# Performance work log

Hardware: AMD Instinct MI355X
Metric: run time of the kernel (lower is better)

The kernel has to match this reference:

```python
import jax, jax.numpy as jnp
import numpy as np

E = 1024
H = 16
DH = E // H
LN_EPS = 1e-5


def setup_inputs() -> dict:
    key = jax.random.key(0)
    ks = jax.random.split(key, 9)
    B, Lq, Lk = 8, 1024, 1024
    s = 0.02
    return {
        "query": jax.random.normal(ks[0], (B, Lq, E), jnp.float32),
        "key_t": jax.random.normal(ks[1], (B, Lk, E), jnp.float32),
        "value": jax.random.normal(ks[2], (B, Lk, E), jnp.float32),
        "in_proj_w": jax.random.normal(ks[3], (3 * E, E), jnp.float32) * s,
        "in_proj_b": jnp.zeros((3 * E,), jnp.float32),
        "out_proj_w": jax.random.normal(ks[4], (E, E), jnp.float32) * s,
        "out_proj_b": jnp.zeros((E,), jnp.float32),
        "ln_gamma": jnp.ones((E,), jnp.float32),
        "ln_beta": jnp.zeros((E,), jnp.float32),
    }


def _mha_cross(query, key_t, value, in_proj_w, in_proj_b, out_proj_w, out_proj_b,
               ln_gamma, ln_beta):
    B, Lq, _ = query.shape
    Lk = key_t.shape[1]
    wq, wk, wv = in_proj_w[:E], in_proj_w[E:2 * E], in_proj_w[2 * E:]
    bq, bk, bv = in_proj_b[:E], in_proj_b[E:2 * E], in_proj_b[2 * E:]
    # projections (torch Linear: x @ W^T + b)
    q = (query @ wq.T + bq).reshape(B, Lq, H, DH)
    k = (key_t @ wk.T + bk).reshape(B, Lk, H, DH)
    v = (value @ wv.T + bv).reshape(B, Lk, H, DH)
    scale = 1.0 / np.sqrt(DH).astype(np.float32)
    # unfused attention: explicit [B,H,Lq,Lk] scores (need_weights=True path)
    scores = jnp.einsum("bqhd,bkhd->bhqk", q, k) * scale
    probs = jax.nn.softmax(scores, axis=-1)
    attn = jnp.einsum("bhqk,bkhd->bqhd", probs, v).reshape(B, Lq, E)
    attn_out = attn @ out_proj_w.T + out_proj_b
    # averaged attention weights (average_attn_weights=True default)
    attn_weights = probs.mean(axis=1)  # [B, Lq, Lk]
    # residual + LayerNorm
    x = query + attn_out
    mu = x.mean(axis=-1, keepdims=True)
    var = x.var(axis=-1, keepdims=True)
    y = (x - mu) * jax.lax.rsqrt(var + LN_EPS) * ln_gamma + ln_beta
    return y, attn_weights


def reference(query, key_t, value, in_proj_w, in_proj_b, out_proj_w, out_proj_b,
              ln_gamma, ln_beta):
    return _mha_cross(query, key_t, value, in_proj_w, in_proj_b,
                      out_proj_w, out_proj_b, ln_gamma, ln_beta)
```

## Files before the change

kernel.cpp:

```cpp
#include <hip/hip_runtime.h>
#include <stdint.h>

#define E_DIM 1024
#define H_NUM 16
#define B_NUM 8
#define LQ 1024
#define LK 1024
#define MROWS (B_NUM * LQ)

typedef unsigned short u16;
typedef __attribute__((ext_vector_type(8))) short bf16x8;
typedef __attribute__((ext_vector_type(4))) short bf16x4;
typedef __attribute__((ext_vector_type(4))) float f32x4;
typedef bf16x8 __attribute__((may_alias)) bf16x8_ma;
typedef bf16x4 __attribute__((may_alias)) bf16x4_ma;

typedef __attribute__((address_space(1))) const void* gas_ptr;
typedef __attribute__((address_space(3))) void* las_ptr;

__device__ __forceinline__ void gload16(const void* g, void* l) {
  __builtin_amdgcn_global_load_lds((gas_ptr)g, (las_ptr)l, 16, 0, 0);
}

__device__ __forceinline__ u16 f2bf(float f) {
  union { float f; uint32_t u; } c; c.f = f;
  return (u16)((c.u + 0x7FFFu + ((c.u >> 16) & 1u)) >> 16);
}

#define MFMA_BF16(a, b, c) __builtin_amdgcn_mfma_f32_16x16x32_bf16((a), (b), (c), 0, 0, 0)

#define SCALE_Q 0.18033688011112042f

__global__ __launch_bounds__(256) void cvt_f32_bf16(const float* __restrict__ src,
                                                    u16* __restrict__ dst, int n4) {
  int i = blockIdx.x * 256 + threadIdx.x;
  const int stride = gridDim.x * 256;
  for (; i < n4; i += stride) {
    float4 v = ((const float4*)src)[i];
    ushort4 o;
    o.x = f2bf(v.x); o.y = f2bf(v.y); o.z = f2bf(v.z); o.w = f2bf(v.w);
    ((ushort4*)dst)[i] = o;
  }
}

__global__ __launch_bounds__(256) void cvt3_f32_bf16(
    const float* __restrict__ a0, const float* __restrict__ a1, const float* __restrict__ a2,
    u16* __restrict__ o0, u16* __restrict__ o1, u16* __restrict__ o2, int n4) {
  const float* s = (blockIdx.y == 0) ? a0 : (blockIdx.y == 1 ? a1 : a2);
  u16* d = (blockIdx.y == 0) ? o0 : (blockIdx.y == 1 ? o1 : o2);
  int i = blockIdx.x * 256 + threadIdx.x;
  const int stride = gridDim.x * 256;
  for (; i < n4; i += stride) {
    float4 v = ((const float4*)s)[i];
    ushort4 o;
    o.x = f2bf(v.x); o.y = f2bf(v.y); o.z = f2bf(v.z); o.w = f2bf(v.w);
    ((ushort4*)d)[i] = o;
  }
}

template <int MODE>
__global__ __launch_bounds__(256) void gemm_bt(
    const u16* __restrict__ A0, const u16* __restrict__ A1, const u16* __restrict__ A2,
    const u16* __restrict__ W, const float* __restrict__ bias,
    const float* __restrict__ resid,
    u16* __restrict__ outb, float* __restrict__ outf,
    int N, int K, int nwg_n, int nwg_m) {
  __shared__ u16 As[128 * 64];
  __shared__ u16 Bs[128 * 64];

  const int tid = threadIdx.x;
  const int wave = tid >> 6;
  const int lane = tid & 63;
  const int lr = lane & 15, lg = lane >> 4;
  const int wr = wave >> 1, wc = wave & 1;

  const int cpx = (int)gridDim.x >> 3;
  const int bid = blockIdx.x;
  const int wg = (bid & 7) * cpx + (bid >> 3);
  const int n_i = wg % nwg_n;
  const int rest = wg / nwg_n;
  const int m_i = rest % nwg_m;
  const int z = rest / nwg_m;

  const int m0 = m_i * 128;
  const int n0 = n_i * 128;

  const u16* Az = (z == 0) ? A0 : (z == 1 ? A1 : A2);
  const u16* Wz = W + (size_t)z * N * K;
  const float* bs = bias + z * N;
  const float scale = (MODE == 0 && z == 0) ? SCALE_Q : 1.0f;

  const f32x4 fzero = {0.f, 0.f, 0.f, 0.f};
  f32x4 acc[4][4];
#pragma unroll
  for (int a = 0; a < 4; ++a)
#pragma unroll
    for (int b = 0; b < 4; ++b) acc[a][b] = fzero;

  const int lrow8 = lane >> 3;
  const int lcol8 = (lane & 7) * 8;

  for (int kt = 0; kt < K; kt += 64) {
#pragma unroll
    for (int i = 0; i < 4; ++i) {
      const int seg = i * 4 + wave;
      gload16(Wz + (size_t)(n0 + seg * 8 + lrow8) * K + kt + lcol8, &Bs[seg * 512]);
      gload16(Az + (size_t)(m0 + seg * 8 + lrow8) * K + kt + lcol8, &As[seg * 512]);
    }
    __syncthreads();

#pragma unroll
    for (int kk = 0; kk < 64; kk += 32) {
      bf16x8 av[4], bv[4];
#pragma unroll
      for (int t = 0; t < 4; ++t)
        av[t] = *(const bf16x8*)&As[(wr * 64 + t * 16 + lr) * 64 + kk + lg * 8];
#pragma unroll
      for (int t = 0; t < 4; ++t)
        bv[t] = *(const bf16x8*)&Bs[(wc * 64 + t * 16 + lr) * 64 + kk + lg * 8];
#pragma unroll
      for (int mi = 0; mi < 4; ++mi)
#pragma unroll
        for (int ni = 0; ni < 4; ++ni)
          acc[mi][ni] = MFMA_BF16(av[mi], bv[ni], acc[mi][ni]);
    }
    __syncthreads();
  }

  float bvv[4];
#pragma unroll
  for (int ni = 0; ni < 4; ++ni) bvv[ni] = bs[n0 + wc * 64 + ni * 16 + lr];

  if (MODE == 0) {
    u16* Cb = outb + (size_t)z * (size_t)MROWS * N;
#pragma unroll
    for (int mi = 0; mi < 4; ++mi) {
#pragma unroll
      for (int i = 0; i < 4; ++i) {
        const size_t m = (size_t)(m0 + wr * 64 + mi * 16 + lg * 4 + i);
#pragma unroll
        for (int ni = 0; ni < 4; ++ni) {
          const int n = n0 + wc * 64 + ni * 16 + lr;
          Cb[m * N + n] = f2bf((acc[mi][ni][i] + bvv[ni]) * scale);
        }
      }
    }
  } else {
#pragma unroll
    for (int mi = 0; mi < 4; ++mi) {
#pragma unroll
      for (int i = 0; i < 4; ++i) {
        const size_t m = (size_t)(m0 + wr * 64 + mi * 16 + lg * 4 + i);
#pragma unroll
        for (int ni = 0; ni < 4; ++ni) {
          const int n = n0 + wc * 64 + ni * 16 + lr;
          outf[m * N + n] = acc[mi][ni][i] + bvv[ni] + resid[m * N + n];
        }
      }
    }
  }
}

__global__ __launch_bounds__(256) void transpose_v(const u16* __restrict__ Vb,
                                                   u16* __restrict__ Vtg) {
  __shared__ u16 T[64 * 264];
  const int tid = threadIdx.x;
  const int b = blockIdx.z, h = blockIdx.y;
  const int k0 = blockIdx.x * 256;
  const int bh = b * H_NUM + h;
  const int krow = tid >> 3;
  const int d0 = (tid & 7) * 8;
  const int jst = krow & 7;
#pragma unroll
  for (int it = 0; it < 8; ++it) {
    const int k = it * 32 + krow;
    bf16x8 v = *(const bf16x8*)&Vb[(size_t)(b * LK + k0 + k) * E_DIM + h * 64 + d0];
#pragma unroll
    for (int jj = 0; jj < 8; ++jj) {
      const int j = (jj + jst) & 7;
      T[(d0 + j) * 264 + k] = (u16)v[j];
    }
  }
  __syncthreads();
  const int d = tid >> 2;
  const int kk0 = (tid & 3) * 64;
  u16* orow = &Vtg[(size_t)(bh * 64 + d) * LK + k0 + kk0];
#pragma unroll
  for (int c = 0; c < 8; ++c)
    *(bf16x8*)&orow[c * 8] = *(const bf16x8*)&T[d * 264 + kk0 + c * 8];
}

__global__ __launch_bounds__(256) void attn_fwd(
    const u16* __restrict__ Qb, const u16* __restrict__ Kb, const u16* __restrict__ Vtg,
    u16* __restrict__ attnb, float* __restrict__ denom) {
  __shared__ u16 Ks[64 * 72];
  __shared__ u16 Vt[64 * 72];
  __shared__ u16 Pw[4][16 * 72];

  const int tid = threadIdx.x;
  const int wave = tid >> 6, lane = tid & 63;
  const int lr = lane & 15, lg = lane >> 4;

  const int bid = blockIdx.x;
  const int wg = (bid & 7) * 256 + (bid >> 3);
  const int qt = wg & 15;
  const int h = (wg >> 4) & 15;
  const int b = wg >> 8;
  const int bh = b * H_NUM + h;
  const int q0 = qt * 64;

  const size_t qoff = (size_t)(b * LQ + q0 + wave * 16 + lr) * E_DIM + h * 64;
  const bf16x8 qf0 = *(const bf16x8*)&Qb[qoff + lg * 8];
  const bf16x8 qf1 = *(const bf16x8*)&Qb[qoff + 32 + lg * 8];

  const f32x4 fzero = {0.f, 0.f, 0.f, 0.f};
  f32x4 ctx[4];
#pragma unroll
  for (int d = 0; d < 4; ++d) ctx[d] = fzero;
  float dnl = 0.f;

  const int sr = tid >> 2;
  const int sc = (tid & 3) * 16;
  const u16* Kg = &Kb[(size_t)(b * LK + sr) * E_DIM + h * 64 + sc];
  const u16* Vg = &Vtg[(size_t)(bh * 64 + sr) * LK + sc];

  bf16x8 kr0 = *(const bf16x8*)(Kg);
  bf16x8 kr1 = *(const bf16x8*)(Kg + 8);
  bf16x8 vr0 = *(const bf16x8*)(Vg);
  bf16x8 vr1 = *(const bf16x8*)(Vg + 8);
  *(bf16x8*)&Ks[sr * 72 + sc] = kr0; *(bf16x8*)&Ks[sr * 72 + sc + 8] = kr1;
  *(bf16x8*)&Vt[sr * 72 + sc] = vr0; *(bf16x8*)&Vt[sr * 72 + sc + 8] = vr1;

  for (int t = 0; t < 16; ++t) {
    __syncthreads();
    if (t < 15) {
      const int k1 = (t + 1) * 64;
      kr0 = *(const bf16x8*)(Kg + (size_t)k1 * E_DIM);
      kr1 = *(const bf16x8*)(Kg + (size_t)k1 * E_DIM + 8);
      vr0 = *(const bf16x8*)(Vg + k1);
      vr1 = *(const bf16x8*)(Vg + k1 + 8);
    }
#pragma unroll
    for (int kf = 0; kf < 4; ++kf) {
      const bf16x8 kb0 = *(const bf16x8*)&Ks[(kf * 16 + lr) * 72 + lg * 8];
      const bf16x8 kb1 = *(const bf16x8*)&Ks[(kf * 16 + lr) * 72 + 32 + lg * 8];
      f32x4 s = fzero;
      s = MFMA_BF16(kb0, qf0, s);
      s = MFMA_BF16(kb1, qf1, s);
      const float p0 = exp2f(s[0]), p1 = exp2f(s[1]);
      const float p2 = exp2f(s[2]), p3 = exp2f(s[3]);
      dnl += (p0 + p1) + (p2 + p3);
      bf16x4 w;
      w[0] = (short)f2bf(p0); w[1] = (short)f2bf(p1);
      w[2] = (short)f2bf(p2); w[3] = (short)f2bf(p3);
      *(bf16x4_ma*)&Pw[wave][lr * 72 + kf * 16 + lg * 4] = w;
    }
    const bf16x8 pa0 = *(const bf16x8_ma*)&Pw[wave][lr * 72 + lg * 8];
    const bf16x8 pa1 = *(const bf16x8_ma*)&Pw[wave][lr * 72 + 32 + lg * 8];
#pragma unroll
    for (int df = 0; df < 4; ++df) {
      const bf16x8 vb0 = *(const bf16x8*)&Vt[(df * 16 + lr) * 72 + lg * 8];
      const bf16x8 vb1 = *(const bf16x8*)&Vt[(df * 16 + lr) * 72 + 32 + lg * 8];
      ctx[df] = MFMA_BF16(pa0, vb0, ctx[df]);
      ctx[df] = MFMA_BF16(pa1, vb1, ctx[df]);
    }
    __syncthreads();
    if (t < 15) {
      *(bf16x8*)&Ks[sr * 72 + sc] = kr0; *(bf16x8*)&Ks[sr * 72 + sc + 8] = kr1;
      *(bf16x8*)&Vt[sr * 72 + sc] = vr0; *(bf16x8*)&Vt[sr * 72 + sc + 8] = vr1;
    }
  }

  dnl += __shfl_xor(dnl, 16, 64);
  dnl += __shfl_xor(dnl, 32, 64);
  if (lane < 16) denom[(size_t)bh * LQ + q0 + wave * 16 + lane] = dnl;
  float dnv[4];
#pragma unroll
  for (int i = 0; i < 4; ++i) dnv[i] = __shfl(dnl, lg * 4 + i, 64);

#pragma unroll
  for (int i = 0; i < 4; ++i) {
    const float inv = 1.0f / dnv[i];
    const int q = q0 + wave * 16 + lg * 4 + i;
    const size_t orow = (size_t)(b * LQ + q) * E_DIM + h * 64;
#pragma unroll
    for (int df = 0; df < 4; ++df)
      attnb[orow + df * 16 + lr] = f2bf(ctx[df][i] * inv);
  }
}

__global__ __launch_bounds__(256) void attn_wts(
    const u16* __restrict__ Qb, const u16* __restrict__ Kb,
    const float* __restrict__ denom, float* __restrict__ aw) {
  __shared__ u16 Ks[128 * 72];

  const int tid = threadIdx.x;
  const int wave = tid >> 6, lane = tid & 63;
  const int lr = lane & 15, lg = lane >> 4;

  const int bid = blockIdx.x;
  const int wg = (bid & 7) * 128 + (bid >> 3);
  const int q0 = (wg & 15) * 64;
  const int k0 = ((wg >> 4) & 7) * 128;
  const int b = wg >> 7;

  const f32x4 fzero = {0.f, 0.f, 0.f, 0.f};
  f32x4 acc[2][4];
#pragma unroll
  for (int t = 0; t < 2; ++t)
#pragma unroll
    for (int f = 0; f < 4; ++f) acc[t][f] = fzero;

  const int sr = tid >> 1;
  const int sc = (tid & 1) * 32;
  const u16* Kg = &Kb[(size_t)(b * LK + k0 + sr) * E_DIM + sc];
  const size_t qbase = (size_t)(b * LQ + q0 + wave * 16 + lr) * E_DIM;
  const size_t dbase = (size_t)(b * H_NUM) * LQ + q0 + wave * 16 + lg * 4;

  bf16x8 r0 = *(const bf16x8*)(Kg);
  bf16x8 r1 = *(const bf16x8*)(Kg + 8);
  bf16x8 r2 = *(const bf16x8*)(Kg + 16);
  bf16x8 r3 = *(const bf16x8*)(Kg + 24);
  *(bf16x8*)&Ks[sr * 72 + sc] = r0;      *(bf16x8*)&Ks[sr * 72 + sc + 8] = r1;
  *(bf16x8*)&Ks[sr * 72 + sc + 16] = r2; *(bf16x8*)&Ks[sr * 72 + sc + 24] = r3;

  for (int h = 0; h < H_NUM; ++h) {
    __syncthreads();
    if (h < 15) {
      const u16* Kn = Kg + (h + 1) * 64;
      r0 = *(const bf16x8*)(Kn);
      r1 = *(const bf16x8*)(Kn + 8);
      r2 = *(const bf16x8*)(Kn + 16);
      r3 = *(const bf16x8*)(Kn + 24);
    }
    const bf16x8 qf0 = *(const bf16x8*)&Qb[qbase + h * 64 + lg * 8];
    const bf16x8 qf1 = *(const bf16x8*)&Qb[qbase + h * 64 + 32 + lg * 8];
    float rd[4];
#pragma unroll
    for (int i = 0; i < 4; ++i)
      rd[i] = 0.0625f / denom[dbase + (size_t)h * LQ + i];

#pragma unroll
    for (int kt = 0; kt < 2; ++kt) {
#pragma unroll
      for (int f = 0; f < 4; ++f) {
        const int row = kt * 64 + f * 16 + lr;
        const bf16x8 kb0 = *(const bf16x8*)&Ks[row * 72 + lg * 8];
        const bf16x8 kb1 = *(const bf16x8*)&Ks[row * 72 + 32 + lg * 8];
        f32x4 s = fzero;
        s = MFMA_BF16(qf0, kb0, s);
        s = MFMA_BF16(qf1, kb1, s);
#pragma unroll
        for (int i = 0; i < 4; ++i)
          acc[kt][f][i] += exp2f(s[i]) * rd[i];
      }
    }
    __syncthreads();
    if (h < 15) {
      *(bf16x8*)&Ks[sr * 72 + sc] = r0;      *(bf16x8*)&Ks[sr * 72 + sc + 8] = r1;
      *(bf16x8*)&Ks[sr * 72 + sc + 16] = r2; *(bf16x8*)&Ks[sr * 72 + sc + 24] = r3;
    }
  }

#pragma unroll
  for (int kt = 0; kt < 2; ++kt)
#pragma unroll
    for (int f = 0; f < 4; ++f)
#pragma unroll
      for (int i = 0; i < 4; ++i) {
        const int q = q0 + wave * 16 + lg * 4 + i;
        aw[(size_t)(b * LQ + q) * LK + k0 + kt * 64 + f * 16 + lr] = acc[kt][f][i];
      }
}

__global__ __launch_bounds__(256) void ln_kernel(float* __restrict__ xy,
                                                 const float* __restrict__ gamma,
                                                 const float* __restrict__ beta) {
  __shared__ float ls[4], ls2[4];
  const int row = blockIdx.x;
  const int tid = threadIdx.x;
  float4* xr = (float4*)(xy + (size_t)row * E_DIM);
  float4 v = xr[tid];
  float s = v.x + v.y + v.z + v.w;
  float s2 = v.x * v.x + v.y * v.y + v.z * v.z + v.w * v.w;
#pragma unroll
  for (int off = 32; off >= 1; off >>= 1) {
    s += __shfl_xor(s, off, 64);
    s2 += __shfl_xor(s2, off, 64);
  }
  const int wave = tid >> 6, lane = tid & 63;
  if (lane == 0) { ls[wave] = s; ls2[wave] = s2; }
  __syncthreads();
  s = ls[0] + ls[1] + ls[2] + ls[3];
  s2 = ls2[0] + ls2[1] + ls2[2] + ls2[3];
  const float mu = s * (1.0f / E_DIM);
  const float var = s2 * (1.0f / E_DIM) - mu * mu;
  const float rs = rsqrtf(var + 1e-5f);
  const float4 g = ((const float4*)gamma)[tid];
  const float4 bt = ((const float4*)beta)[tid];
  float4 o;
  o.x = (v.x - mu) * rs * g.x + bt.x;
  o.y = (v.y - mu) * rs * g.y + bt.y;
  o.z = (v.z - mu) * rs * g.z + bt.z;
  o.w = (v.w - mu) * rs * g.w + bt.w;
  xr[tid] = o;
}

extern "C" void kernel_launch(void* const* d_in, const int* in_sizes, int n_in,
                              void* d_out, int out_size, void* d_ws, size_t ws_size,
                              hipStream_t stream) {
  (void)in_sizes; (void)n_in; (void)out_size; (void)ws_size;
  const float* query     = (const float*)d_in[0];
  const float* key_t     = (const float*)d_in[1];
  const float* value     = (const float*)d_in[2];
  const float* in_proj_b = (const float*)d_in[4];
  const float* out_proj_b = (const float*)d_in[6];
  const float* ln_gamma  = (const float*)d_in[7];
  const float* ln_beta   = (const float*)d_in[8];

  float* y  = (float*)d_out;
  float* aw = y + (size_t)B_NUM * LQ * E_DIM;

  const size_t SZ = (size_t)B_NUM * LQ * E_DIM;
  u16* ws    = (u16*)d_ws;
  u16* Qb    = ws;
  u16* Kb    = ws + SZ;
  u16* Vb    = ws + 2 * SZ;
  u16* attnb = ws + 3 * SZ;
  u16* wqkvb = ws + 4 * SZ;
  u16* woutb = wqkvb + 3 * E_DIM * E_DIM;
  float* denom = (float*)(wqkvb + 4 * (size_t)E_DIM * E_DIM);

  u16* Xq  = (u16*)aw;
  u16* Xk  = Xq + SZ;
  u16* Xv  = (u16*)y;
  u16* Vtg = (u16*)y;

  cvt_f32_bf16<<<3072, 256, 0, stream>>>((const float*)d_in[3], wqkvb, (3 * E_DIM * E_DIM) / 4);
  cvt_f32_bf16<<<1024, 256, 0, stream>>>((const float*)d_in[5], woutb, (E_DIM * E_DIM) / 4);
  cvt3_f32_bf16<<<dim3(2048, 3), 256, 0, stream>>>(query, key_t, value, Xq, Xk, Xv, (int)(SZ / 4));

  gemm_bt<0><<<1536, 256, 0, stream>>>(
      Xq, Xk, Xv, wqkvb, in_proj_b, nullptr, Qb, nullptr, E_DIM, E_DIM, 8, 64);

  transpose_v<<<dim3(4, 16, 8), 256, 0, stream>>>(Vb, Vtg);

  attn_fwd<<<2048, 256, 0, stream>>>(Qb, Kb, Vtg, attnb, denom);

  attn_wts<<<1024, 256, 0, stream>>>(Qb, Kb, denom, aw);

  gemm_bt<1><<<512, 256, 0, stream>>>(
      attnb, attnb, attnb, woutb, out_proj_b, query, nullptr, y, E_DIM, E_DIM, 8, 64);

  ln_kernel<<<8192, 256, 0, stream>>>(y, ln_gamma, ln_beta);
}
```

Baseline: 309.1 us.

## Replace 128x128 GEMM with pipelined 256x256 tile, swizzled LDS, 8 waves

Replaces the projection and output GEMMs with a 256x256-tile, 512-thread kernel. It double-buffers K=64 slices in 128KB of LDS with an XOR-swizzled layout, and interleaves async global-to-LDS loads with MFMA phases, using explicit waitcnt, barriers and setprio. The aim is to raise arithmetic intensity and hide load latency behind the matrix ops. In exchange the out-projection launches only 128 workgroups, which may underfill the GPU, and the fine-grained barrier and waitcnt choreography is fragile.

```diff
diff --git a/kernel.cpp b/kernel.cpp
--- a/kernel.cpp
+++ b/kernel.cpp
@@ -58,21 +58,56 @@
   }
 }
 
+
+#define BAR() __builtin_amdgcn_s_barrier()
+#define LGKM0() do { asm volatile("s_waitcnt lgkmcnt(0)" ::: "memory"); \
+                     __builtin_amdgcn_sched_barrier(0); } while (0)
+#define LGKM8() asm volatile("s_waitcnt lgkmcnt(8)" ::: "memory")
+#define VMC(n) asm volatile("s_waitcnt vmcnt(" n ")" ::: "memory")
+
+#define STAGEH(mat, rowbase, kt, ldsoff)                                     \
+  { const u16* _s = (mat) + (size_t)(rowbase) * E_DIM + (kt);                \
+    gload16(_s + goff0, ldsv + (ldsoff) + wave * 1024);                      \
+    gload16(_s + goff1, ldsv + (ldsoff) + 8192 + wave * 1024); }
+
+#define READ_B(db)                                                           \
+  _Pragma("unroll") for (int n = 0; n < 4; ++n) {                            \
+    const int rgb = wn4 + n;                                                 \
+    _Pragma("unroll") for (int ks = 0; ks < 2; ++ks)                         \
+      bfr[n][ks] = *(const bf16x8_ma*)(ldsc + 65536 + (db) * 32768 +         \
+          ((rgb >> 3) << 14) + (((rgb & 7) * 2 + ks) << 10) + lanebase);     \
+  }
+
+#define READ_A(db, q)                                                        \
+  _Pragma("unroll") for (int jj = 0; jj < 2; ++jj) {                         \
+    const int rga = 4 * (q) + 2 * jj + wm;                                   \
+    _Pragma("unroll") for (int ks = 0; ks < 2; ++ks)                         \
+      afr[jj][ks] = *(const bf16x8_ma*)(ldsc + (db) * 32768 +                \
+          ((rga >> 3) << 14) + (((rga & 7) * 2 + ks) << 10) + lanebase);     \
+  }
+
+#define MMA(q)                                                               \
+  __builtin_amdgcn_s_setprio(1);                                             \
+  _Pragma("unroll") for (int jj = 0; jj < 2; ++jj)                           \
+    _Pragma("unroll") for (int n = 0; n < 4; ++n)                            \
+      _Pragma("unroll") for (int ks = 0; ks < 2; ++ks)                       \
+        acc[2 * (q) + jj][n] =                                               \
+            MFMA_BF16(afr[jj][ks], bfr[n][ks], acc[2 * (q) + jj][n]);        \
+  __builtin_amdgcn_s_setprio(0);
+
 template <int MODE>
-__global__ __launch_bounds__(256) void gemm_bt(
+__global__ __launch_bounds__(512, 2) void gemm256(
     const u16* __restrict__ A0, const u16* __restrict__ A1, const u16* __restrict__ A2,
     const u16* __restrict__ W, const float* __restrict__ bias,
     const float* __restrict__ resid,
     u16* __restrict__ outb, float* __restrict__ outf,
-    int N, int K, int nwg_n, int nwg_m) {
-  __shared__ u16 As[128 * 64];
-  __shared__ u16 Bs[128 * 64];
+    int nwg_n, int nwg_m) {
+  __shared__ u16 lds[65536];
 
   const int tid = threadIdx.x;
-  const int wave = tid >> 6;
-  const int lane = tid & 63;
+  const int wave = tid >> 6, lane = tid & 63;
   const int lr = lane & 15, lg = lane >> 4;
-  const int wr = wave >> 1, wc = wave & 1;
+  const int wm = wave >> 2, wn4 = (wave & 3) * 4;
 
   const int cpx = (int)gridDim.x >> 3;
   const int bid = blockIdx.x;
@@ -81,80 +116,132 @@
   const int rest = wg / nwg_n;
   const int m_i = rest % nwg_m;
   const int z = rest / nwg_m;
-
-  const int m0 = m_i * 128;
-  const int n0 = n_i * 128;
+  const int m0 = m_i * 256, n0 = n_i * 256;
 
   const u16* Az = (z == 0) ? A0 : (z == 1 ? A1 : A2);
-  const u16* Wz = W + (size_t)z * N * K;
-  const float* bs = bias + z * N;
+  const u16* Wz = W + (size_t)z * E_DIM * E_DIM;
+  const float* bs = bias + z * E_DIM;
   const float scale = (MODE == 0 && z == 0) ? SCALE_Q : 1.0f;
 
+  int goff0, goff1;
+  {
+    const int X0 = wave * 1024 + lane * 16;
+    const int L0 = X0 ^ (((X0 >> 9) & 1) << 5);
+    goff0 = (((L0 >> 10) >> 1) * 16 + ((L0 >> 6) & 15)) * E_DIM +
+            ((L0 >> 10) & 1) * 32 + ((L0 & 63) >> 1);
+    const int X1 = 8192 + X0;
+    const int L1 = X1 ^ (((X1 >> 9) & 1) << 5);
+    goff1 = (((L1 >> 10) >> 1) * 16 + ((L1 >> 6) & 15)) * E_DIM +
+            ((L1 >> 10) & 1) * 32 + ((L1 & 63) >> 1);
+  }
+  const char* ldsc = (const char*)lds;
+  char* ldsv = (char*)lds;
+  const int lanebase = lr * 64 + ((lg * 16) ^ ((lane & 8) << 2));
+
   const f32x4 fzero = {0.f, 0.f, 0.f, 0.f};
-  f32x4 acc[4][4];
-#pragma unroll
-  for (int a = 0; a < 4; ++a)
-#pragma unroll
-    for (int b = 0; b < 4; ++b) acc[a][b] = fzero;
-
-  const int lrow8 = lane >> 3;
-  const int lcol8 = (lane & 7) * 8;
-
-  for (int kt = 0; kt < K; kt += 64) {
-#pragma unroll
-    for (int i = 0; i < 4; ++i) {
-      const int seg = i * 4 + wave;
-      gload16(Wz + (size_t)(n0 + seg * 8 + lrow8) * K + kt + lcol8, &Bs[seg * 512]);
-      gload16(Az + (size_t)(m0 + seg * 8 + lrow8) * K + kt + lcol8, &As[seg * 512]);
-    }
-    __syncthreads();
-
-#pragma unroll
-    for (int kk = 0; kk < 64; kk += 32) {
-      bf16x8 av[4], bv[4];
-#pragma unroll
-      for (int t = 0; t < 4; ++t)
-        av[t] = *(const bf16x8*)&As[(wr * 64 + t * 16 + lr) * 64 + kk + lg * 8];
-#pragma unroll
-      for (int t = 0; t < 4; ++t)
-        bv[t] = *(const bf16x8*)&Bs[(wc * 64 + t * 16 + lr) * 64 + kk + lg * 8];
-#pragma unroll
-      for (int mi = 0; mi < 4; ++mi)
-#pragma unroll
-        for (int ni = 0; ni < 4; ++ni)
-          acc[mi][ni] = MFMA_BF16(av[mi], bv[ni], acc[mi][ni]);
-    }
-    __syncthreads();
+  f32x4 acc[8][4];
+#pragma unroll
+  for (int j = 0; j < 8; ++j)
+#pragma unroll
+    for (int n = 0; n < 4; ++n) acc[j][n] = fzero;
+
+  STAGEH(Az, m0,       0,  0);
+  STAGEH(Az, m0 + 128, 0,  16384);
+  STAGEH(Wz, n0,       0,  65536);
+  STAGEH(Wz, n0 + 128, 0,  65536 + 16384);
+  STAGEH(Wz, n0,       64, 65536 + 32768);
+  STAGEH(Wz, n0 + 128, 64, 65536 + 32768 + 16384);
+  STAGEH(Az, m0,       64, 32768);
+  VMC("6");
+  BAR();
+
+  bf16x8 bfr[4][2], afr[2][2];
+#pragma unroll 1
+  for (int i = 0; i < 8; ++i) {
+    const int kt2 = i * 128 + 128;
+    const bool nl = (i < 7);
+    READ_B(0) READ_A(0, 0)
+    STAGEH(Az, m0 + 128, i * 128 + 64, 32768 + 16384);
+    LGKM8();
+    BAR(); LGKM0();
+    MMA(0)
+    BAR();
+    READ_A(0, 1)
+    if (nl) STAGEH(Wz, n0, kt2, 65536);
+    BAR(); LGKM0();
+    MMA(1)
+    BAR();
+    READ_A(0, 2)
+    if (nl) STAGEH(Az, m0, kt2, 0);
+    BAR(); LGKM0();
+    MMA(2)
+    BAR();
+    READ_A(0, 3)
+    if (nl) {
+      STAGEH(Wz, n0 + 128, kt2, 65536 + 16384);
+      VMC("6");
+    } else {
+      VMC("0");
+    }
+    BAR(); LGKM0();
+    MMA(3)
+    BAR();
+    READ_B(1) READ_A(1, 0)
+    if (nl) STAGEH(Az, m0 + 128, kt2, 16384);
+    LGKM8();
+    BAR(); LGKM0();
+    MMA(0)
+    BAR();
+    READ_A(1, 1)
+    if (nl) STAGEH(Wz, n0, kt2 + 64, 65536 + 32768);
+    BAR(); LGKM0();
+    MMA(1)
+    BAR();
+    READ_A(1, 2)
+    if (nl) STAGEH(Wz, n0 + 128, kt2 + 64, 65536 + 32768 + 16384);
+    BAR(); LGKM0();
+    MMA(2)
+    BAR();
+    READ_A(1, 3)
+    if (nl) {
+      STAGEH(Az, m0, kt2 + 64, 32768);
+      VMC("6");
+    }
+    BAR(); LGKM0();
+    MMA(3)
+    BAR();
   }
 
   float bvv[4];
 #pragma unroll
-  for (int ni = 0; ni < 4; ++ni) bvv[ni] = bs[n0 + wc * 64 + ni * 16 + lr];
+  for (int n = 0; n < 4; ++n) bvv[n] = bs[n0 + wn4 * 16 + n * 16 + lr];
 
   if (MODE == 0) {
-    u16* Cb = outb + (size_t)z * (size_t)MROWS * N;
-#pragma unroll
-    for (int mi = 0; mi < 4; ++mi) {
-#pragma unroll
-      for (int i = 0; i < 4; ++i) {
-        const size_t m = (size_t)(m0 + wr * 64 + mi * 16 + lg * 4 + i);
-#pragma unroll
-        for (int ni = 0; ni < 4; ++ni) {
-          const int n = n0 + wc * 64 + ni * 16 + lr;
-          Cb[m * N + n] = f2bf((acc[mi][ni][i] + bvv[ni]) * scale);
+    u16* Cb = outb + (size_t)z * (size_t)MROWS * E_DIM;
+#pragma unroll
+    for (int j = 0; j < 8; ++j) {
+      const int rbase = m0 + (2 * j + wm) * 16 + lg * 4;
+#pragma unroll
+      for (int ii = 0; ii < 4; ++ii) {
+        const size_t m = (size_t)(rbase + ii);
+#pragma unroll
+        for (int n = 0; n < 4; ++n) {
+          const int nn = n0 + wn4 * 16 + n * 16 + lr;
+          Cb[m * E_DIM + nn] = f2bf((acc[j][n][ii] + bvv[n]) * scale);
         }
       }
     }
   } else {
 #pragma unroll
-    for (int mi = 0; mi < 4; ++mi) {
-#pragma unroll
-      for (int i = 0; i < 4; ++i) {
-        const size_t m = (size_t)(m0 + wr * 64 + mi * 16 + lg * 4 + i);
-#pragma unroll
-        for (int ni = 0; ni < 4; ++ni) {
-          const int n = n0 + wc * 64 + ni * 16 + lr;
-          outf[m * N + n] = acc[mi][ni][i] + bvv[ni] + resid[m * N + n];
+    for (int j = 0; j < 8; ++j) {
+      const int rbase = m0 + (2 * j + wm) * 16 + lg * 4;
+#pragma unroll
+      for (int ii = 0; ii < 4; ++ii) {
+        const size_t m = (size_t)(rbase + ii);
+#pragma unroll
+        for (int n = 0; n < 4; ++n) {
+          const int nn = n0 + wn4 * 16 + n * 16 + lr;
+          outf[m * E_DIM + nn] = acc[j][n][ii] + bvv[n] + resid[m * E_DIM + nn];
         }
       }
     }
@@ -440,8 +527,8 @@
   cvt_f32_bf16<<<1024, 256, 0, stream>>>((const float*)d_in[5], woutb, (E_DIM * E_DIM) / 4);
   cvt3_f32_bf16<<<dim3(2048, 3), 256, 0, stream>>>(query, key_t, value, Xq, Xk, Xv, (int)(SZ / 4));
 
-  gemm_bt<0><<<1536, 256, 0, stream>>>(
-      Xq, Xk, Xv, wqkvb, in_proj_b, nullptr, Qb, nullptr, E_DIM, E_DIM, 8, 64);
+  gemm256<0><<<384, 512, 0, stream>>>(
+      Xq, Xk, Xv, wqkvb, in_proj_b, nullptr, Qb, nullptr, 4, 32);
 
   transpose_v<<<dim3(4, 16, 8), 256, 0, stream>>>(Vb, Vtg);
 
@@ -449,8 +536,8 @@
 
   attn_wts<<<1024, 256, 0, stream>>>(Qb, Kb, denom, aw);
 
-  gemm_bt<1><<<512, 256, 0, stream>>>(
-      attnb, attnb, attnb, woutb, out_proj_b, query, nullptr, y, E_DIM, E_DIM, 8, 64);
+  gemm256<1><<<128, 512, 0, stream>>>(
+      attnb, attnb, attnb, woutb, out_proj_b, query, nullptr, y, 4, 32);
 
   ln_kernel<<<8192, 256, 0, stream>>>(y, ln_gamma, ln_beta);
 }
```

Result: faster. 294.9 us (-4.6%).
